# Kernel tuning notes

Hardware: AMD Instinct MI355X
Metric: run time of the kernel (lower is better)

## Reference

```python
import jax, jax.numpy as jnp
import numpy as np

N = 40000      # nodes
E = 640000     # edges (avg degree 16)
D_IN = 256     # input_size
H = 128        # hidden_size
C = 64         # num_classes
L = 2          # num_middle_layers


def spmm(val, row, col, mat):
    # sparse [N,N] @ dense [N,D]: gather neighbor rows, scale, scatter-add
    return jax.ops.segment_sum(val[:, None] * mat[col], row, num_segments=mat.shape[0])


def setup_inputs() -> dict:
    key = jax.random.key(0)
    ks = jax.random.split(key, 12)
    x = jax.random.normal(ks[0], (N, D_IN), dtype=jnp.float32)
    edge_row = jax.random.randint(ks[1], (E,), 0, N)
    edge_col = jax.random.randint(ks[2], (E,), 0, N)
    edge_val = jax.random.uniform(ks[3], (E,), dtype=jnp.float32) / 16.0  # ~normalized adjacency
    # Linear params (stored [in, out]; math equivalent to torch x @ W.T + b)
    w1 = jax.random.normal(ks[4], (D_IN, H), dtype=jnp.float32) * (1.0 / np.sqrt(D_IN))
    b1 = jax.random.normal(ks[5], (H,), dtype=jnp.float32) * 0.01
    wm = jax.random.normal(ks[6], (L, H, H), dtype=jnp.float32) * (1.0 / np.sqrt(H))
    bm = jax.random.normal(ks[7], (L, H), dtype=jnp.float32) * 0.01
    w2 = jax.random.normal(ks[8], (H, C), dtype=jnp.float32) * (1.0 / np.sqrt(H))
    b2 = jax.random.normal(ks[9], (C,), dtype=jnp.float32) * 0.01
    time_step = jnp.array(0.1, dtype=jnp.float32)
    return {"x": x, "edge_row": edge_row, "edge_col": edge_col, "edge_val": edge_val,
            "w1": w1, "b1": b1, "wm": wm, "bm": bm, "w2": w2, "b2": b2,
            "time_step": time_step}


def reference(x, edge_row, edge_col, edge_val, w1, b1, wm, bm, w2, b2, time_step):
    # dropout p=0 -> identity
    h = jax.nn.relu(spmm(edge_val, edge_row, edge_col, x @ w1 + b1))
    for i in range(L):  # residual middle layers: x <- x + relu(A @ (x W + b)) * dt
        f = jax.nn.relu(spmm(edge_val, edge_row, edge_col, h @ wm[i] + bm[i]))
        h = h + f * time_step
    return spmm(edge_val, edge_row, edge_col, h @ w2 + b2)
```

## Files before the change

kernel.cpp:

```cpp
#include <hip/hip_runtime.h>


#define DIN 256
#define HID 128
#define NCLS 64

typedef __attribute__((ext_vector_type(8))) short bf16x8;
typedef __attribute__((ext_vector_type(4))) float f32x4;

static __device__ __forceinline__ float bf2f(unsigned int u) {
    return __uint_as_float(u << 16);
}
static __device__ __forceinline__ unsigned short f2bf(float f) {
    unsigned int i = __float_as_uint(f);
    unsigned int r = (i + 0x7FFFu + ((i >> 16) & 1u)) >> 16;
    return (unsigned short)r;
}
static __device__ __forceinline__ unsigned int pack2(float a, float b) {
    return (unsigned int)f2bf(a) | ((unsigned int)f2bf(b) << 16);
}


__global__ void hist_kernel(const int* __restrict__ row, int* __restrict__ deg, int E) {
    int e = blockIdx.x * blockDim.x + threadIdx.x;
    if (e < E) atomicAdd(&deg[row[e]], 1);
}

__global__ __launch_bounds__(1024) void scan_sums_kernel(
        const int* __restrict__ deg, int* __restrict__ bsums, int n) {
    __shared__ int wsum[16];
    const int lane = threadIdx.x & 63;
    const int wid  = threadIdx.x >> 6;
    int i = blockIdx.x * 1024 + threadIdx.x;
    int v = (i < n) ? deg[i] : 0;
    #pragma unroll
    for (int d = 32; d >= 1; d >>= 1) v += __shfl_xor(v, d, 64);
    if (lane == 0) wsum[wid] = v;
    __syncthreads();
    if (threadIdx.x == 0) {
        int s = 0;
        #pragma unroll
        for (int w = 0; w < 16; ++w) s += wsum[w];
        bsums[blockIdx.x] = s;
    }
}

__global__ __launch_bounds__(1024) void scan_fix_kernel(
        const int* __restrict__ deg, const int* __restrict__ bsums,
        int* __restrict__ offs, int* __restrict__ pos, int n, int nb) {
    __shared__ int wsum[16];
    __shared__ int bpref_s;
    const int lane = threadIdx.x & 63;
    const int wid  = threadIdx.x >> 6;
    const int b = blockIdx.x;
    if (wid == 0) {
        int v = (lane < nb && lane < b) ? bsums[lane] : 0;
        #pragma unroll
        for (int d = 32; d >= 1; d >>= 1) v += __shfl_xor(v, d, 64);
        if (lane == 0) bpref_s = v;
    }
    int i = b * 1024 + (int)threadIdx.x;
    int v = (i < n) ? deg[i] : 0;
    int incl = v;
    #pragma unroll
    for (int d = 1; d < 64; d <<= 1) {
        int t = __shfl_up(incl, d, 64);
        if (lane >= d) incl += t;
    }
    if (lane == 63) wsum[wid] = incl;
    __syncthreads();
    int wpref = 0;
    #pragma unroll
    for (int w = 0; w < 16; ++w)
        if (w < wid) wpref += wsum[w];
    int excl = bpref_s + wpref + incl - v;
    if (i < n) { offs[i] = excl; pos[i] = excl; }
    if (i == n) offs[n] = excl;
}

__global__ void wtrans_all_kernel(const float* __restrict__ w1, const float* __restrict__ wm,
                                  const float* __restrict__ w2,
                                  unsigned short* __restrict__ w1t, unsigned short* __restrict__ wmt,
                                  unsigned short* __restrict__ w2t, int L) {
    int idx = blockIdx.x * blockDim.x + threadIdx.x;
    int n1 = DIN * HID;
    int n2 = n1 + L * HID * HID;
    int n3 = n2 + HID * NCLS;
    if (idx < n1) {
        int n = idx / DIN, k = idx - n * DIN;
        w1t[idx] = f2bf(w1[(size_t)k * HID + n]);
    } else if (idx < n2) {
        int j = idx - n1;
        int i = j / (HID * HID), r = j - i * (HID * HID);
        int n = r / HID, k = r - n * HID;
        wmt[j] = f2bf(wm[(size_t)i * HID * HID + (size_t)k * HID + n]);
    } else if (idx < n3) {
        int j = idx - n2;
        int n = j / HID, k = j - n * HID;
        w2t[j] = f2bf(w2[(size_t)k * NCLS + n]);
    }
}

__global__ __launch_bounds__(256) void mega1_kernel(
        const float* __restrict__ x, const unsigned short* __restrict__ w1t,
        const float* __restrict__ b1, unsigned short* __restrict__ z,
        const int* __restrict__ erow, const int* __restrict__ ecol,
        const float* __restrict__ eval, int* __restrict__ pos,
        int2* __restrict__ edges, int E, int gemmBlocks) {
    const int tid = threadIdx.x;
    if ((int)blockIdx.x >= gemmBlocks) {
        int nfb = gridDim.x - gemmBlocks;
        for (int e = (blockIdx.x - gemmBlocks) * 256 + tid; e < E; e += nfb * 256) {
            int r = erow[e];
            int p = atomicAdd(&pos[r], 1);
            int2 o;
            o.x = ecol[e];
            o.y = __float_as_int(eval[e]);
            edges[p] = o;
        }
        return;
    }
    __shared__ __align__(16) unsigned short Alds[64 * 40];
    __shared__ __align__(16) unsigned short Blds[128 * 40];
    const int bm   = blockIdx.x * 64;
    const int wave = tid >> 6;
    const int lane = tid & 63;
    const int m16  = lane & 15;
    const int quad = lane >> 4;
    const int ar = tid >> 2, ac = (tid & 3) * 8;

    f32x4 acc[8] = {};
    for (int k0 = 0; k0 < DIN; k0 += 32) {
        float4 a0 = *(const float4*)&x[(size_t)(bm + ar) * DIN + k0 + ac];
        float4 a1 = *(const float4*)&x[(size_t)(bm + ar) * DIN + k0 + ac + 4];
        uint4 av;
        av.x = pack2(a0.x, a0.y); av.y = pack2(a0.z, a0.w);
        av.z = pack2(a1.x, a1.y); av.w = pack2(a1.z, a1.w);
        *(uint4*)&Alds[ar * 40 + ac] = av;
        #pragma unroll
        for (int i = 0; i < 2; ++i) {
            int c  = tid + 256 * i;
            int br = c >> 2, bc = (c & 3) * 8;
            *(uint4*)&Blds[br * 40 + bc] = *(const uint4*)&w1t[(size_t)br * DIN + k0 + bc];
        }
        __syncthreads();
        bf16x8 af = *(const bf16x8*)&Alds[(wave * 16 + m16) * 40 + quad * 8];
        #pragma unroll
        for (int j = 0; j < 8; ++j) {
            bf16x8 bf = *(const bf16x8*)&Blds[(j * 16 + m16) * 40 + quad * 8];
            acc[j] = __builtin_amdgcn_mfma_f32_16x16x32_bf16(af, bf, acc[j], 0, 0, 0);
        }
        __syncthreads();
    }
    #pragma unroll
    for (int j = 0; j < 8; ++j) {
        int col = j * 16 + m16;
        float bb = b1[col];
        #pragma unroll
        for (int r = 0; r < 4; ++r) {
            int row = bm + wave * 16 + quad * 4 + r;
            z[(size_t)row * HID + col] = f2bf(acc[j][r] + bb);
        }
    }
}

template <int BN>
__global__ __launch_bounds__(256) void gemm_mfma_kernel(
        const unsigned short* __restrict__ A, const unsigned short* __restrict__ Wt,
        const float* __restrict__ bias, unsigned short* __restrict__ C, int K) {
    constexpr int NT = BN / 16;
    __shared__ __align__(16) unsigned short Alds[64 * 40];
    __shared__ __align__(16) unsigned short Blds[BN * 40];
    const int tid  = threadIdx.x;
    const int bm   = blockIdx.x * 64;
    const int wave = tid >> 6;
    const int lane = tid & 63;
    const int m16  = lane & 15;
    const int quad = lane >> 4;
    const int ar = tid >> 2, ac = (tid & 3) * 8;

    f32x4 acc[NT] = {};
    for (int k0 = 0; k0 < K; k0 += 32) {
        uint4 av = *(const uint4*)&A[(size_t)(bm + ar) * K + k0 + ac];
        *(uint4*)&Alds[ar * 40 + ac] = av;
        #pragma unroll
        for (int i = 0; i < BN / 64; ++i) {
            int c  = tid + 256 * i;
            int br = c >> 2, bc = (c & 3) * 8;
            *(uint4*)&Blds[br * 40 + bc] = *(const uint4*)&Wt[(size_t)br * K + k0 + bc];
        }
        __syncthreads();
        bf16x8 af = *(const bf16x8*)&Alds[(wave * 16 + m16) * 40 + quad * 8];
        #pragma unroll
        for (int j = 0; j < NT; ++j) {
            bf16x8 bf = *(const bf16x8*)&Blds[(j * 16 + m16) * 40 + quad * 8];
            acc[j] = __builtin_amdgcn_mfma_f32_16x16x32_bf16(af, bf, acc[j], 0, 0, 0);
        }
        __syncthreads();
    }
    #pragma unroll
    for (int j = 0; j < NT; ++j) {
        int col = j * 16 + m16;
        float bb = bias[col];
        #pragma unroll
        for (int r = 0; r < 4; ++r) {
            int row = bm + wave * 16 + quad * 4 + r;
            C[(size_t)row * BN + col] = f2bf(acc[j][r] + bb);
        }
    }
}

template <int D, int MODE>
__global__ __launch_bounds__(256) void spmm_kernel(
        const int* __restrict__ offs, const int2* __restrict__ edges,
        const unsigned short* __restrict__ z,
        float* __restrict__ out, unsigned short* __restrict__ hb,
        const float* __restrict__ dt_ptr, int n) {
    int r = (int)((blockIdx.x * blockDim.x + threadIdx.x) >> 6);
    int lane = threadIdx.x & 63;
    if (r >= n) return;
    r = __builtin_amdgcn_readfirstlane(r);
    const int s = offs[r], e = offs[r + 1];
    float acc0 = 0.f, acc1 = 0.f;
    int p = s;
    if (D == 128) {
        const unsigned int* z32 = (const unsigned int*)z;
        for (; p + 4 <= e; p += 4) {
            int2 e0 = edges[p], e1 = edges[p + 1], e2 = edges[p + 2], e3 = edges[p + 3];
            unsigned int g0 = z32[(size_t)e0.x * 64 + lane];
            unsigned int g1 = z32[(size_t)e1.x * 64 + lane];
            unsigned int g2 = z32[(size_t)e2.x * 64 + lane];
            unsigned int g3 = z32[(size_t)e3.x * 64 + lane];
            float v0 = __int_as_float(e0.y), v1 = __int_as_float(e1.y);
            float v2 = __int_as_float(e2.y), v3 = __int_as_float(e3.y);
            acc0 = fmaf(v0, bf2f(g0 & 0xffffu), acc0); acc1 = fmaf(v0, bf2f(g0 >> 16), acc1);
            acc0 = fmaf(v1, bf2f(g1 & 0xffffu), acc0); acc1 = fmaf(v1, bf2f(g1 >> 16), acc1);
            acc0 = fmaf(v2, bf2f(g2 & 0xffffu), acc0); acc1 = fmaf(v2, bf2f(g2 >> 16), acc1);
            acc0 = fmaf(v3, bf2f(g3 & 0xffffu), acc0); acc1 = fmaf(v3, bf2f(g3 >> 16), acc1);
        }
        for (; p < e; ++p) {
            int2 ed = edges[p];
            float v = __int_as_float(ed.y);
            unsigned int g = z32[(size_t)ed.x * 64 + lane];
            acc0 = fmaf(v, bf2f(g & 0xffffu), acc0); acc1 = fmaf(v, bf2f(g >> 16), acc1);
        }
        float2* op = (float2*)&out[(size_t)r * 128 + 2 * lane];
        float f0, f1;
        if (MODE == 0) {
            f0 = fmaxf(acc0, 0.f); f1 = fmaxf(acc1, 0.f);
            float2 o; o.x = f0; o.y = f1; *op = o;
        } else if (MODE == 1) {
            float dt = *dt_ptr;
            float2 cur = *op;
            f0 = cur.x + fmaxf(acc0, 0.f) * dt;
            f1 = cur.y + fmaxf(acc1, 0.f) * dt;
            float2 o; o.x = f0; o.y = f1; *op = o;
        } else {
            float2 o; o.x = acc0; o.y = acc1; *op = o;
            return;
        }
        ((unsigned int*)hb)[(size_t)r * 64 + lane] = pack2(f0, f1);
    } else {
        for (; p + 4 <= e; p += 4) {
            int2 e0 = edges[p], e1 = edges[p + 1], e2 = edges[p + 2], e3 = edges[p + 3];
            unsigned int g0 = z[(size_t)e0.x * 64 + lane];
            unsigned int g1 = z[(size_t)e1.x * 64 + lane];
            unsigned int g2 = z[(size_t)e2.x * 64 + lane];
            unsigned int g3 = z[(size_t)e3.x * 64 + lane];
            acc0 = fmaf(__int_as_float(e0.y), bf2f(g0), acc0);
            acc0 = fmaf(__int_as_float(e1.y), bf2f(g1), acc0);
            acc0 = fmaf(__int_as_float(e2.y), bf2f(g2), acc0);
            acc0 = fmaf(__int_as_float(e3.y), bf2f(g3), acc0);
        }
        for (; p < e; ++p) {
            int2 ed = edges[p];
            acc0 = fmaf(__int_as_float(ed.y), bf2f((unsigned int)z[(size_t)ed.x * 64 + lane]), acc0);
        }
        out[(size_t)r * 64 + lane] = acc0;
    }
}

extern "C" void kernel_launch(void* const* d_in, const int* in_sizes, int n_in,
                              void* d_out, int out_size, void* d_ws, size_t ws_size,
                              hipStream_t stream) {
    const float* x    = (const float*)d_in[0];
    const int*   erow = (const int*)d_in[1];
    const int*   ecol = (const int*)d_in[2];
    const float* eval = (const float*)d_in[3];
    const float* w1   = (const float*)d_in[4];
    const float* b1   = (const float*)d_in[5];
    const float* wm   = (const float*)d_in[6];
    const float* bmp  = (const float*)d_in[7];
    const float* w2   = (const float*)d_in[8];
    const float* b2   = (const float*)d_in[9];
    const float* dt   = (const float*)d_in[10];

    const int N = in_sizes[0] / DIN;
    const int E = in_sizes[1];
    const int L = in_sizes[7] / HID;

    float* outp = (float*)d_out;

    char* ws = (char*)d_ws;
    auto carve = [&](size_t bytes) -> char* {
        char* p = ws;
        ws += (bytes + 255) & ~(size_t)255;
        return p;
    };
    int*            deg   = (int*)carve((size_t)N * 4);
    int*            bsums = (int*)carve(64 * 4);
    int*            offs  = (int*)carve((size_t)(N + 1) * 4);
    int*            pos   = (int*)carve((size_t)N * 4);
    int2*           edges = (int2*)carve((size_t)E * 8);
    unsigned short* z     = (unsigned short*)carve((size_t)N * HID * 2);
    float*          h     = (float*)carve((size_t)N * HID * 4);
    unsigned short* hb    = (unsigned short*)carve((size_t)N * HID * 2);
    unsigned short* w1t   = (unsigned short*)carve((size_t)HID * DIN * 2);
    unsigned short* wmt   = (unsigned short*)carve((size_t)L * HID * HID * 2);
    unsigned short* w2t   = (unsigned short*)carve((size_t)NCLS * HID * 2);

    const int ntiles = (N + 1024) / 1024;
    const int wtotal = DIN * HID + L * HID * HID + HID * NCLS;

    wtrans_all_kernel<<<(wtotal + 255) / 256, 256, 0, stream>>>(w1, wm, w2, w1t, wmt, w2t, L);
    hipMemsetAsync(deg, 0, (size_t)N * 4, stream);
    hist_kernel<<<(E + 255) / 256, 256, 0, stream>>>(erow, deg, E);
    scan_sums_kernel<<<ntiles, 1024, 0, stream>>>(deg, bsums, N);
    scan_fix_kernel<<<ntiles, 1024, 0, stream>>>(deg, bsums, offs, pos, N, ntiles);

    const int gemm_blocks = N / 64;
    const int spmm_blocks = (N + 3) / 4;

    mega1_kernel<<<gemm_blocks * 2, 256, 0, stream>>>(
        x, w1t, b1, z, erow, ecol, eval, pos, edges, E, gemm_blocks);
    spmm_kernel<HID, 0><<<spmm_blocks, 256, 0, stream>>>(offs, edges, z, h, hb, nullptr, N);

    for (int i = 0; i < L; ++i) {
        gemm_mfma_kernel<HID><<<gemm_blocks, 256, 0, stream>>>(
            hb, wmt + (size_t)i * HID * HID, bmp + (size_t)i * HID, z, HID);
        spmm_kernel<HID, 1><<<spmm_blocks, 256, 0, stream>>>(offs, edges, z, h, hb, dt, N);
    }

    gemm_mfma_kernel<NCLS><<<gemm_blocks, 256, 0, stream>>>(hb, w2t, b2, z, HID);
    spmm_kernel<NCLS, 2><<<spmm_blocks, 256, 0, stream>>>(offs, edges, z, outp, nullptr, nullptr, N);
}
```

Measured before the change: 299.4 us.

## Partition histogram/edge-fill atomics by row range; unroll SpMM gathers by 8 with nontemporal loads

The histogram and CSR fill kernels now run 8 row-range partitions, each block scanning a strided share of all edges and doing atomics only for rows in its partition. The likely aim is atomic locality, with each partition's counters fitting a smaller footprint, likely grouped by block index across XCDs. In exchange every edge row index is read 8 times. The SpMM inner loop is unrolled to 8 edges with separate load phases to raise memory-level parallelism, and uses nontemporal loads for edge records and nontemporal stores for hb. The hardcoded 78 stride assumes exactly 624 fill blocks and depends on gemm_blocks being a multiple of 8 for the part mapping.

```diff
diff --git a/kernel.cpp b/kernel.cpp
--- a/kernel.cpp
+++ b/kernel.cpp
@@ -21,9 +21,17 @@
 }
 
 
-__global__ void hist_kernel(const int* __restrict__ row, int* __restrict__ deg, int E) {
-    int e = blockIdx.x * blockDim.x + threadIdx.x;
-    if (e < E) atomicAdd(&deg[row[e]], 1);
+__global__ __launch_bounds__(256) void hist_kernel(
+        const int* __restrict__ row, int* __restrict__ deg, int E, int chunk, int N) {
+    const int part = blockIdx.x & 7;
+    const int rp   = blockIdx.x >> 3;
+    const int lo = part * chunk;
+    const int hi = min(lo + chunk, N);
+    for (int e = rp * 256 + (int)threadIdx.x; e < E; e += 78 * 256) {
+        int r = row[e];
+        if ((unsigned)(r - lo) < (unsigned)(hi - lo))
+            atomicAdd(&deg[r], 1);
+    }
 }
 
 __global__ __launch_bounds__(1024) void scan_sums_kernel(
@@ -106,17 +114,21 @@
         const float* __restrict__ b1, unsigned short* __restrict__ z,
         const int* __restrict__ erow, const int* __restrict__ ecol,
         const float* __restrict__ eval, int* __restrict__ pos,
-        int2* __restrict__ edges, int E, int gemmBlocks) {
+        long long* __restrict__ edges, int E, int chunk, int N, int gemmBlocks) {
     const int tid = threadIdx.x;
     if ((int)blockIdx.x >= gemmBlocks) {
-        int nfb = gridDim.x - gemmBlocks;
-        for (int e = (blockIdx.x - gemmBlocks) * 256 + tid; e < E; e += nfb * 256) {
+        const int fb   = blockIdx.x - gemmBlocks;
+        const int part = blockIdx.x & 7;
+        const int rp   = fb >> 3;
+        const int lo = part * chunk;
+        const int hi = min(lo + chunk, N);
+        for (int e = rp * 256 + tid; e < E; e += 78 * 256) {
             int r = erow[e];
-            int p = atomicAdd(&pos[r], 1);
-            int2 o;
-            o.x = ecol[e];
-            o.y = __float_as_int(eval[e]);
-            edges[p] = o;
+            if ((unsigned)(r - lo) < (unsigned)(hi - lo)) {
+                int p = atomicAdd(&pos[r], 1);
+                long long o = ((long long)__float_as_int(eval[e]) << 32) | (unsigned int)ecol[e];
+                edges[p] = o;
+            }
         }
         return;
     }
@@ -212,7 +224,7 @@
 
 template <int D, int MODE>
 __global__ __launch_bounds__(256) void spmm_kernel(
-        const int* __restrict__ offs, const int2* __restrict__ edges,
+        const int* __restrict__ offs, const long long* __restrict__ edges,
         const unsigned short* __restrict__ z,
         float* __restrict__ out, unsigned short* __restrict__ hb,
         const float* __restrict__ dt_ptr, int n) {
@@ -225,24 +237,27 @@
     int p = s;
     if (D == 128) {
         const unsigned int* z32 = (const unsigned int*)z;
-        for (; p + 4 <= e; p += 4) {
-            int2 e0 = edges[p], e1 = edges[p + 1], e2 = edges[p + 2], e3 = edges[p + 3];
-            unsigned int g0 = z32[(size_t)e0.x * 64 + lane];
-            unsigned int g1 = z32[(size_t)e1.x * 64 + lane];
-            unsigned int g2 = z32[(size_t)e2.x * 64 + lane];
-            unsigned int g3 = z32[(size_t)e3.x * 64 + lane];
-            float v0 = __int_as_float(e0.y), v1 = __int_as_float(e1.y);
-            float v2 = __int_as_float(e2.y), v3 = __int_as_float(e3.y);
-            acc0 = fmaf(v0, bf2f(g0 & 0xffffu), acc0); acc1 = fmaf(v0, bf2f(g0 >> 16), acc1);
-            acc0 = fmaf(v1, bf2f(g1 & 0xffffu), acc0); acc1 = fmaf(v1, bf2f(g1 >> 16), acc1);
-            acc0 = fmaf(v2, bf2f(g2 & 0xffffu), acc0); acc1 = fmaf(v2, bf2f(g2 >> 16), acc1);
-            acc0 = fmaf(v3, bf2f(g3 & 0xffffu), acc0); acc1 = fmaf(v3, bf2f(g3 >> 16), acc1);
+        for (; p + 8 <= e; p += 8) {
+            long long ev[8];
+            unsigned int g[8];
+            #pragma unroll
+            for (int i = 0; i < 8; ++i) ev[i] = __builtin_nontemporal_load(edges + p + i);
+            #pragma unroll
+            for (int i = 0; i < 8; ++i)
+                g[i] = z32[(size_t)(int)((unsigned int)ev[i]) * 64 + lane];
+            #pragma unroll
+            for (int i = 0; i < 8; ++i) {
+                float v = __int_as_float((int)(ev[i] >> 32));
+                acc0 = fmaf(v, bf2f(g[i] & 0xffffu), acc0);
+                acc1 = fmaf(v, bf2f(g[i] >> 16), acc1);
+            }
         }
         for (; p < e; ++p) {
-            int2 ed = edges[p];
-            float v = __int_as_float(ed.y);
-            unsigned int g = z32[(size_t)ed.x * 64 + lane];
-            acc0 = fmaf(v, bf2f(g & 0xffffu), acc0); acc1 = fmaf(v, bf2f(g >> 16), acc1);
+            long long ev = __builtin_nontemporal_load(edges + p);
+            float v = __int_as_float((int)(ev >> 32));
+            unsigned int g = z32[(size_t)(int)((unsigned int)ev) * 64 + lane];
+            acc0 = fmaf(v, bf2f(g & 0xffffu), acc0);
+            acc1 = fmaf(v, bf2f(g >> 16), acc1);
         }
         float2* op = (float2*)&out[(size_t)r * 128 + 2 * lane];
         float f0, f1;
@@ -259,22 +274,24 @@
             float2 o; o.x = acc0; o.y = acc1; *op = o;
             return;
         }
-        ((unsigned int*)hb)[(size_t)r * 64 + lane] = pack2(f0, f1);
+        __builtin_nontemporal_store(pack2(f0, f1), (unsigned int*)hb + (size_t)r * 64 + lane);
     } else {
-        for (; p + 4 <= e; p += 4) {
-            int2 e0 = edges[p], e1 = edges[p + 1], e2 = edges[p + 2], e3 = edges[p + 3];
-            unsigned int g0 = z[(size_t)e0.x * 64 + lane];
-            unsigned int g1 = z[(size_t)e1.x * 64 + lane];
-            unsigned int g2 = z[(size_t)e2.x * 64 + lane];
-            unsigned int g3 = z[(size_t)e3.x * 64 + lane];
-            acc0 = fmaf(__int_as_float(e0.y), bf2f(g0), acc0);
-            acc0 = fmaf(__int_as_float(e1.y), bf2f(g1), acc0);
-            acc0 = fmaf(__int_as_float(e2.y), bf2f(g2), acc0);
-            acc0 = fmaf(__int_as_float(e3.y), bf2f(g3), acc0);
+        for (; p + 8 <= e; p += 8) {
+            long long ev[8];
+            unsigned int g[8];
+            #pragma unroll
+            for (int i = 0; i < 8; ++i) ev[i] = __builtin_nontemporal_load(edges + p + i);
+            #pragma unroll
+            for (int i = 0; i < 8; ++i)
+                g[i] = z[(size_t)(int)((unsigned int)ev[i]) * 64 + lane];
+            #pragma unroll
+            for (int i = 0; i < 8; ++i)
+                acc0 = fmaf(__int_as_float((int)(ev[i] >> 32)), bf2f(g[i]), acc0);
         }
         for (; p < e; ++p) {
-            int2 ed = edges[p];
-            acc0 = fmaf(__int_as_float(ed.y), bf2f((unsigned int)z[(size_t)ed.x * 64 + lane]), acc0);
+            long long ev = __builtin_nontemporal_load(edges + p);
+            acc0 = fmaf(__int_as_float((int)(ev >> 32)),
+                        bf2f((unsigned int)z[(size_t)(int)((unsigned int)ev) * 64 + lane]), acc0);
         }
         out[(size_t)r * 64 + lane] = acc0;
     }
@@ -298,6 +315,7 @@
     const int N = in_sizes[0] / DIN;
     const int E = in_sizes[1];
     const int L = in_sizes[7] / HID;
+    const int chunk = (N + 7) / 8;
 
     float* outp = (float*)d_out;
 
@@ -311,7 +329,7 @@
     int*            bsums = (int*)carve(64 * 4);
     int*            offs  = (int*)carve((size_t)(N + 1) * 4);
     int*            pos   = (int*)carve((size_t)N * 4);
-    int2*           edges = (int2*)carve((size_t)E * 8);
+    long long*      edges = (long long*)carve((size_t)E * 8);
     unsigned short* z     = (unsigned short*)carve((size_t)N * HID * 2);
     float*          h     = (float*)carve((size_t)N * HID * 4);
     unsigned short* hb    = (unsigned short*)carve((size_t)N * HID * 2);
@@ -324,15 +342,15 @@
 
     wtrans_all_kernel<<<(wtotal + 255) / 256, 256, 0, stream>>>(w1, wm, w2, w1t, wmt, w2t, L);
     hipMemsetAsync(deg, 0, (size_t)N * 4, stream);
-    hist_kernel<<<(E + 255) / 256, 256, 0, stream>>>(erow, deg, E);
+    hist_kernel<<<624, 256, 0, stream>>>(erow, deg, E, chunk, N);
     scan_sums_kernel<<<ntiles, 1024, 0, stream>>>(deg, bsums, N);
     scan_fix_kernel<<<ntiles, 1024, 0, stream>>>(deg, bsums, offs, pos, N, ntiles);
 
     const int gemm_blocks = N / 64;
     const int spmm_blocks = (N + 3) / 4;
 
-    mega1_kernel<<<gemm_blocks * 2, 256, 0, stream>>>(
-        x, w1t, b1, z, erow, ecol, eval, pos, edges, E, gemm_blocks);
+    mega1_kernel<<<gemm_blocks + 624, 256, 0, stream>>>(
+        x, w1t, b1, z, erow, ecol, eval, pos, edges, E, chunk, N, gemm_blocks);
     spmm_kernel<HID, 0><<<spmm_blocks, 256, 0, stream>>>(offs, edges, z, h, hb, nullptr, N);
 
     for (int i = 0; i < L; ++i) {
```

New measurement: 311.3 us. 1.04x slower.

## Store activations in 32-column slices and split SpMM by feature slice

Applied to the files above, without the earlier changes.

GEMM outputs and the bf16 hidden state are written in a column-sliced layout: each block of 32 columns is stored contiguously across all nodes. The SpMM is restructured so that each block handles one slice, with half a wave per row. The intent is that consecutive blocks gather from a smaller slice working set that fits better in cache. In exchange, the edge list is re-read once per slice (using nontemporal loads), each gathered access is narrower (64 bytes per neighbor), and GEMM stores and loads now go through the sliced indexing.

```diff
diff --git a/kernel.cpp b/kernel.cpp
--- a/kernel.cpp
+++ b/kernel.cpp
@@ -106,16 +106,14 @@
         const float* __restrict__ b1, unsigned short* __restrict__ z,
         const int* __restrict__ erow, const int* __restrict__ ecol,
         const float* __restrict__ eval, int* __restrict__ pos,
-        int2* __restrict__ edges, int E, int gemmBlocks) {
+        long long* __restrict__ edges, int E, int N, int gemmBlocks) {
     const int tid = threadIdx.x;
     if ((int)blockIdx.x >= gemmBlocks) {
         int nfb = gridDim.x - gemmBlocks;
         for (int e = (blockIdx.x - gemmBlocks) * 256 + tid; e < E; e += nfb * 256) {
             int r = erow[e];
             int p = atomicAdd(&pos[r], 1);
-            int2 o;
-            o.x = ecol[e];
-            o.y = __float_as_int(eval[e]);
+            long long o = ((long long)__float_as_int(eval[e]) << 32) | (unsigned int)ecol[e];
             edges[p] = o;
         }
         return;
@@ -156,10 +154,11 @@
     for (int j = 0; j < 8; ++j) {
         int col = j * 16 + m16;
         float bb = b1[col];
+        size_t sbase = (size_t)(col >> 5) * N * 32 + (col & 31);
         #pragma unroll
         for (int r = 0; r < 4; ++r) {
             int row = bm + wave * 16 + quad * 4 + r;
-            z[(size_t)row * HID + col] = f2bf(acc[j][r] + bb);
+            z[sbase + (size_t)row * 32] = f2bf(acc[j][r] + bb);
         }
     }
 }
@@ -167,7 +166,7 @@
 template <int BN>
 __global__ __launch_bounds__(256) void gemm_mfma_kernel(
         const unsigned short* __restrict__ A, const unsigned short* __restrict__ Wt,
-        const float* __restrict__ bias, unsigned short* __restrict__ C, int K) {
+        const float* __restrict__ bias, unsigned short* __restrict__ C, int K, int N) {
     constexpr int NT = BN / 16;
     __shared__ __align__(16) unsigned short Alds[64 * 40];
     __shared__ __align__(16) unsigned short Blds[BN * 40];
@@ -181,7 +180,7 @@
 
     f32x4 acc[NT] = {};
     for (int k0 = 0; k0 < K; k0 += 32) {
-        uint4 av = *(const uint4*)&A[(size_t)(bm + ar) * K + k0 + ac];
+        uint4 av = *(const uint4*)&A[(size_t)(k0 >> 5) * N * 32 + (size_t)(bm + ar) * 32 + ac];
         *(uint4*)&Alds[ar * 40 + ac] = av;
         #pragma unroll
         for (int i = 0; i < BN / 64; ++i) {
@@ -202,81 +201,65 @@
     for (int j = 0; j < NT; ++j) {
         int col = j * 16 + m16;
         float bb = bias[col];
+        size_t sbase = (size_t)(col >> 5) * N * 32 + (col & 31);
         #pragma unroll
         for (int r = 0; r < 4; ++r) {
             int row = bm + wave * 16 + quad * 4 + r;
-            C[(size_t)row * BN + col] = f2bf(acc[j][r] + bb);
+            C[sbase + (size_t)row * 32] = f2bf(acc[j][r] + bb);
         }
     }
 }
 
 template <int D, int MODE>
-__global__ __launch_bounds__(256) void spmm_kernel(
-        const int* __restrict__ offs, const int2* __restrict__ edges,
-        const unsigned short* __restrict__ z,
-        float* __restrict__ out, unsigned short* __restrict__ hb,
-        const float* __restrict__ dt_ptr, int n) {
-    int r = (int)((blockIdx.x * blockDim.x + threadIdx.x) >> 6);
-    int lane = threadIdx.x & 63;
-    if (r >= n) return;
-    r = __builtin_amdgcn_readfirstlane(r);
+__global__ __launch_bounds__(256) void spmm_sliced_kernel(
+        const int* __restrict__ offs, const long long* __restrict__ edges,
+        const unsigned short* __restrict__ zs,
+        float* __restrict__ hout, unsigned short* __restrict__ hb,
+        const float* __restrict__ dt_ptr, int N) {
+    constexpr int NS = D / 32;
+    const int sliceId = blockIdx.x & (NS - 1);
+    const int rblk    = blockIdx.x / NS;
+    const int wave = threadIdx.x >> 6;
+    const int lane = threadIdx.x & 63;
+    const int grp  = lane >> 5;
+    const int c    = lane & 31;
+    const int r = rblk * 8 + wave * 2 + grp;
+    if (r >= N) return;
     const int s = offs[r], e = offs[r + 1];
-    float acc0 = 0.f, acc1 = 0.f;
+    const unsigned short* zb = zs + (size_t)sliceId * N * 32 + c;
+    float acc = 0.f;
     int p = s;
-    if (D == 128) {
-        const unsigned int* z32 = (const unsigned int*)z;
-        for (; p + 4 <= e; p += 4) {
-            int2 e0 = edges[p], e1 = edges[p + 1], e2 = edges[p + 2], e3 = edges[p + 3];
-            unsigned int g0 = z32[(size_t)e0.x * 64 + lane];
-            unsigned int g1 = z32[(size_t)e1.x * 64 + lane];
-            unsigned int g2 = z32[(size_t)e2.x * 64 + lane];
-            unsigned int g3 = z32[(size_t)e3.x * 64 + lane];
-            float v0 = __int_as_float(e0.y), v1 = __int_as_float(e1.y);
-            float v2 = __int_as_float(e2.y), v3 = __int_as_float(e3.y);
-            acc0 = fmaf(v0, bf2f(g0 & 0xffffu), acc0); acc1 = fmaf(v0, bf2f(g0 >> 16), acc1);
-            acc0 = fmaf(v1, bf2f(g1 & 0xffffu), acc0); acc1 = fmaf(v1, bf2f(g1 >> 16), acc1);
-            acc0 = fmaf(v2, bf2f(g2 & 0xffffu), acc0); acc1 = fmaf(v2, bf2f(g2 >> 16), acc1);
-            acc0 = fmaf(v3, bf2f(g3 & 0xffffu), acc0); acc1 = fmaf(v3, bf2f(g3 >> 16), acc1);
-        }
-        for (; p < e; ++p) {
-            int2 ed = edges[p];
-            float v = __int_as_float(ed.y);
-            unsigned int g = z32[(size_t)ed.x * 64 + lane];
-            acc0 = fmaf(v, bf2f(g & 0xffffu), acc0); acc1 = fmaf(v, bf2f(g >> 16), acc1);
-        }
-        float2* op = (float2*)&out[(size_t)r * 128 + 2 * lane];
-        float f0, f1;
+    for (; p + 4 <= e; p += 4) {
+        long long e0 = __builtin_nontemporal_load(edges + p);
+        long long e1 = __builtin_nontemporal_load(edges + p + 1);
+        long long e2 = __builtin_nontemporal_load(edges + p + 2);
+        long long e3 = __builtin_nontemporal_load(edges + p + 3);
+        unsigned short g0 = zb[(size_t)(unsigned int)e0 * 32];
+        unsigned short g1 = zb[(size_t)(unsigned int)e1 * 32];
+        unsigned short g2 = zb[(size_t)(unsigned int)e2 * 32];
+        unsigned short g3 = zb[(size_t)(unsigned int)e3 * 32];
+        acc = fmaf(__int_as_float((int)(e0 >> 32)), bf2f(g0), acc);
+        acc = fmaf(__int_as_float((int)(e1 >> 32)), bf2f(g1), acc);
+        acc = fmaf(__int_as_float((int)(e2 >> 32)), bf2f(g2), acc);
+        acc = fmaf(__int_as_float((int)(e3 >> 32)), bf2f(g3), acc);
+    }
+    for (; p < e; ++p) {
+        long long ev = __builtin_nontemporal_load(edges + p);
+        acc = fmaf(__int_as_float((int)(ev >> 32)),
+                   bf2f(zb[(size_t)(unsigned int)ev * 32]), acc);
+    }
+    size_t ho = (size_t)r * D + sliceId * 32 + c;
+    if (MODE == 2) {
+        hout[ho] = acc;
+    } else {
+        float f;
         if (MODE == 0) {
-            f0 = fmaxf(acc0, 0.f); f1 = fmaxf(acc1, 0.f);
-            float2 o; o.x = f0; o.y = f1; *op = o;
-        } else if (MODE == 1) {
-            float dt = *dt_ptr;
-            float2 cur = *op;
-            f0 = cur.x + fmaxf(acc0, 0.f) * dt;
-            f1 = cur.y + fmaxf(acc1, 0.f) * dt;
-            float2 o; o.x = f0; o.y = f1; *op = o;
+            f = fmaxf(acc, 0.f);
         } else {
-            float2 o; o.x = acc0; o.y = acc1; *op = o;
-            return;
-        }
-        ((unsigned int*)hb)[(size_t)r * 64 + lane] = pack2(f0, f1);
-    } else {
-        for (; p + 4 <= e; p += 4) {
-            int2 e0 = edges[p], e1 = edges[p + 1], e2 = edges[p + 2], e3 = edges[p + 3];
-            unsigned int g0 = z[(size_t)e0.x * 64 + lane];
-            unsigned int g1 = z[(size_t)e1.x * 64 + lane];
-            unsigned int g2 = z[(size_t)e2.x * 64 + lane];
-            unsigned int g3 = z[(size_t)e3.x * 64 + lane];
-            acc0 = fmaf(__int_as_float(e0.y), bf2f(g0), acc0);
-            acc0 = fmaf(__int_as_float(e1.y), bf2f(g1), acc0);
-            acc0 = fmaf(__int_as_float(e2.y), bf2f(g2), acc0);
-            acc0 = fmaf(__int_as_float(e3.y), bf2f(g3), acc0);
-        }
-        for (; p < e; ++p) {
-            int2 ed = edges[p];
-            acc0 = fmaf(__int_as_float(ed.y), bf2f((unsigned int)z[(size_t)ed.x * 64 + lane]), acc0);
-        }
-        out[(size_t)r * 64 + lane] = acc0;
+            f = hout[ho] + fmaxf(acc, 0.f) * (*dt_ptr);
+        }
+        hout[ho] = f;
+        hb[(size_t)sliceId * N * 32 + (size_t)r * 32 + c] = f2bf(f);
     }
 }
 
@@ -311,7 +294,7 @@
     int*            bsums = (int*)carve(64 * 4);
     int*            offs  = (int*)carve((size_t)(N + 1) * 4);
     int*            pos   = (int*)carve((size_t)N * 4);
-    int2*           edges = (int2*)carve((size_t)E * 8);
+    long long*      edges = (long long*)carve((size_t)E * 8);
     unsigned short* z     = (unsigned short*)carve((size_t)N * HID * 2);
     float*          h     = (float*)carve((size_t)N * HID * 4);
     unsigned short* hb    = (unsigned short*)carve((size_t)N * HID * 2);
@@ -328,19 +311,20 @@
     scan_sums_kernel<<<ntiles, 1024, 0, stream>>>(deg, bsums, N);
     scan_fix_kernel<<<ntiles, 1024, 0, stream>>>(deg, bsums, offs, pos, N, ntiles);
 
-    const int gemm_blocks = N / 64;
-    const int spmm_blocks = (N + 3) / 4;
+    const int gemm_blocks  = N / 64;
+    const int spmm128_blks = (N / 8) * 4;
+    const int spmm64_blks  = (N / 8) * 2;
 
     mega1_kernel<<<gemm_blocks * 2, 256, 0, stream>>>(
-        x, w1t, b1, z, erow, ecol, eval, pos, edges, E, gemm_blocks);
-    spmm_kernel<HID, 0><<<spmm_blocks, 256, 0, stream>>>(offs, edges, z, h, hb, nullptr, N);
+        x, w1t, b1, z, erow, ecol, eval, pos, edges, E, N, gemm_blocks);
+    spmm_sliced_kernel<HID, 0><<<spmm128_blks, 256, 0, stream>>>(offs, edges, z, h, hb, nullptr, N);
 
     for (int i = 0; i < L; ++i) {
         gemm_mfma_kernel<HID><<<gemm_blocks, 256, 0, stream>>>(
-            hb, wmt + (size_t)i * HID * HID, bmp + (size_t)i * HID, z, HID);
-        spmm_kernel<HID, 1><<<spmm_blocks, 256, 0, stream>>>(offs, edges, z, h, hb, dt, N);
-    }
-
-    gemm_mfma_kernel<NCLS><<<gemm_blocks, 256, 0, stream>>>(hb, w2t, b2, z, HID);
-    spmm_kernel<NCLS, 2><<<spmm_blocks, 256, 0, stream>>>(offs, edges, z, outp, nullptr, nullptr, N);
-}
+            hb, wmt + (size_t)i * HID * HID, bmp + (size_t)i * HID, z, HID, N);
+        spmm_sliced_kernel<HID, 1><<<spmm128_blks, 256, 0, stream>>>(offs, edges, z, h, hb, dt, N);
+    }
+
+    gemm_mfma_kernel<NCLS><<<gemm_blocks, 256, 0, stream>>>(hb, w2t, b2, z, HID, N);
+    spmm_sliced_kernel<NCLS, 2><<<spmm64_blks, 256, 0, stream>>>(offs, edges, z, outp, nullptr, nullptr, N);
+}
```

Measured after the change: 478.4 us. +59.8%, slower.
